# Kernel tuning notes

Hardware: AMD Instinct MI355X
Metric: run time of the kernel (lower is better)

The kernel has to match this reference:

```python
import jax, jax.numpy as jnp
import numpy as np

N, D_IN, H, E = 8192, 2048, 1024, 8

def setup_inputs() -> dict:
    key = jax.random.key(0)
    ks = jax.random.split(key, 12)
    s = lambda k, shp, fan: jax.random.normal(k, shp, jnp.float32) * (1.0 / np.sqrt(fan))
    return {
        "x": jax.random.normal(ks[0], (N, D_IN), jnp.float32),
        "enc_W": s(ks[1], (D_IN, H), D_IN),
        "enc_b": jnp.zeros((H,), jnp.float32),
        "gate_W": s(ks[2], (H, E), H),
        "expert_W": s(ks[3], (E, H, H), H),
        "expert_b": jnp.zeros((E, H), jnp.float32),
        "mlp_W": s(ks[4], (H, H), H),
        "mlp_b": jnp.zeros((H,), jnp.float32),
        "coef_W": s(ks[5], (H, 2), H),
        "coef_b": jnp.zeros((2,), jnp.float32),
        "dec_W": s(ks[6], (H, D_IN), H),
        "dec_b": jnp.zeros((D_IN,), jnp.float32),
    }

def reference(x, enc_W, enc_b, gate_W, expert_W, expert_b,
              mlp_W, mlp_b, coef_W, coef_b, dec_W, dec_b):
    # encoder + relu
    h = jax.nn.relu(x @ enc_W + enc_b)                       # [N,H]
    # top-1 gate
    probs = jax.nn.softmax(h @ gate_W, axis=-1)              # [N,E]
    idx = jnp.argmax(probs, axis=-1)                         # [N]
    p = jnp.take_along_axis(probs, idx[:, None], axis=1)     # [N,1]
    onehot = jax.nn.one_hot(idx, probs.shape[-1], dtype=h.dtype)  # [N,E]
    # dispatch -> per-expert GEMM -> combine
    xe = jnp.einsum('ne,nh->enh', onehot, h)                 # [E,N,H]
    ye = jnp.einsum('enh,ehd->end', xe, expert_W) + expert_b[:, None, :]
    moe_out = jnp.einsum('ne,end->nd', onehot, ye) * p       # [N,H]
    # residual MoE mixing
    mlp_out = h @ mlp_W + mlp_b                              # [N,H]
    coef = jax.nn.softmax(h @ coef_W + coef_b, axis=-1)      # [N,2]
    out = moe_out * coef[:, 0:1] + mlp_out * coef[:, 1:2]
    # decoder
    return out @ dec_W + dec_b                               # [N,D_IN]
```

## Files before the change

kernel.cpp:

```cpp
#include <hip/hip_runtime.h>
#include <hip/hip_bf16.h>
#include <stdint.h>


using bf16 = __hip_bfloat16;
typedef __bf16 bf16x8 __attribute__((ext_vector_type(8)));
typedef float f32x4 __attribute__((ext_vector_type(4)));

static constexpr int NROWS = 8192;
static constexpr int DIN   = 2048;
static constexpr int HD    = 1024;
static constexpr int NEXP  = 8;
static constexpr int MAX_TILES = 72;
static constexpr int MAXFLAG  = 512;
static constexpr int MAXFLAG2 = 128;
static constexpr int F1Z = 7;
#define GAPTHR  0.02f
#define GAPTHR2 1.0e-3

__device__ __forceinline__ uint16_t f2u(float f) {
  bf16 h = __float2bfloat16(f);
  uint16_t u; __builtin_memcpy(&u, &h, 2); return u;
}
__device__ __forceinline__ float u2f(uint16_t u) {
  uint32_t x = ((uint32_t)u) << 16;
  float f; __builtin_memcpy(&f, &x, 4); return f;
}

typedef const __attribute__((address_space(1))) void* gas_ptr;
typedef __attribute__((address_space(3))) void* las_ptr;
__device__ __forceinline__ void async16(void* lds, const void* g) {
  __builtin_amdgcn_global_load_lds((gas_ptr)g, (las_ptr)lds, 16, 0, 0);
}

__global__ __launch_bounds__(256)
void prep_kernel(const float* __restrict__ x, uint16_t* __restrict__ x_bf,
                 const float* __restrict__ encW, uint16_t* __restrict__ encWT,
                 const float* __restrict__ mlpW, uint16_t* __restrict__ mlpWT,
                 const float* __restrict__ decW, uint16_t* __restrict__ decWT,
                 const float* __restrict__ expW, uint16_t* __restrict__ expWT,
                 int* __restrict__ ctrs_i)
{
  __shared__ float tile[64 * 65];
  const int b = blockIdx.x;
  const int t = threadIdx.x;
  if (b == 0 && t < 64) ctrs_i[t] = 0;

  if (b < 1024) {
    for (int i = b * 256 + t; i < NROWS * DIN / 8; i += 1024 * 256) {
      const float* s = x + (size_t)i * 8;
      float4 v0 = *(const float4*)(s);
      float4 v1 = *(const float4*)(s + 4);
      uint16_t tmp[8];
      tmp[0]=f2u(v0.x); tmp[1]=f2u(v0.y); tmp[2]=f2u(v0.z); tmp[3]=f2u(v0.w);
      tmp[4]=f2u(v1.x); tmp[5]=f2u(v1.y); tmp[6]=f2u(v1.z); tmp[7]=f2u(v1.w);
      int4 pv; __builtin_memcpy(&pv, tmp, 16);
      *(int4*)(x_bf + (size_t)i * 8) = pv;
    }
    return;
  }
  const float* in; uint16_t* out; int R, C, bx, by;
  int q = b - 1024;
  if (q < 512)       { in = encW; out = encWT; R = DIN; C = HD;  bx = q & 15; by = q >> 4; }
  else if (q < 768)  { q -= 512;  in = mlpW; out = mlpWT; R = HD; C = HD;  bx = q & 15; by = q >> 4; }
  else if (q < 1280) { q -= 768;  in = decW; out = decWT; R = HD; C = DIN; bx = q & 31; by = q >> 5; }
  else { q -= 1280; const int z = q >> 8; q &= 255;
         in = expW + (size_t)z * HD * HD; out = expWT + (size_t)z * HD * HD;
         R = HD; C = HD; bx = q & 15; by = q >> 4; }
  const int C0 = bx * 64, R0 = by * 64;
  const int cl = (t & 7) * 8;
#pragma unroll
  for (int p = 0; p < 2; ++p) {
    const int r = p * 32 + (t >> 3);
    const float* src = in + (size_t)(R0 + r) * C + C0 + cl;
    float4 v0 = *(const float4*)(src);
    float4 v1 = *(const float4*)(src + 4);
    float* dst = &tile[r * 65 + cl];
    dst[0]=v0.x; dst[1]=v0.y; dst[2]=v0.z; dst[3]=v0.w;
    dst[4]=v1.x; dst[5]=v1.y; dst[6]=v1.z; dst[7]=v1.w;
  }
  __syncthreads();
#pragma unroll
  for (int p = 0; p < 2; ++p) {
    const int oc = p * 32 + (t >> 3);
    uint16_t tmp[8];
#pragma unroll
    for (int j = 0; j < 8; ++j) tmp[j] = f2u(tile[(cl + j) * 65 + oc]);
    int4 v; __builtin_memcpy(&v, tmp, 16);
    *(int4*)(out + (size_t)(C0 + oc) * R + R0 + cl) = v;
  }
}

template<int MODE>
__device__ __forceinline__
void gemm8p_body(const uint16_t* __restrict__ A, const uint16_t* __restrict__ BT,
                 uint16_t* __restrict__ C16, float* __restrict__ C32,
                 const float* __restrict__ biasf, const float* __restrict__ scale,
                 int M, int N, int K)
{
  constexpr int BM = 256, BN = 128, BK = 64;
  __shared__ uint16_t As[2][BM * BK];
  __shared__ uint16_t Bs[2][BN * BK];

  const int t = threadIdx.x;
  const int ntyg = gridDim.y;
  const int nwg  = gridDim.x * ntyg;
  const int hwf  = blockIdx.y * gridDim.x + blockIdx.x;
  const int swzb = (hwf & 7) * (nwg >> 3) + (hwf >> 3);
  const int mtile = swzb / ntyg;
  const int ntile = swzb % ntyg;

  const int trow = t >> 3;
  const int cbD  = (t & 7) * 16;
  const int cbS  = cbD ^ ((trow & 7) << 4);
  const char* aRow[4];
  const char* bRow[2];
#pragma unroll
  for (int c = 0; c < 4; ++c)
    aRow[c] = (const char*)A + ((size_t)(mtile * BM + c * 64 + trow) * K) * 2 + cbS;
#pragma unroll
  for (int c = 0; c < 2; ++c)
    bRow[c] = (const char*)BT + ((size_t)(ntile * BN + c * 64 + trow) * K) * 2 + cbS;

  auto stage = [&](int b, int kt) {
#pragma unroll
    for (int c = 0; c < 4; ++c)
      async16(&As[b][c * 4096 + t * 8], aRow[c] + (size_t)kt * 128);
#pragma unroll
    for (int c = 0; c < 2; ++c)
      async16(&Bs[b][c * 4096 + t * 8], bRow[c] + (size_t)kt * 128);
  };

  const int wid = t >> 6, lane = t & 63;
  const int wm = wid >> 2, wn = wid & 3;
  const int frow = lane & 15, hi = lane >> 4;

  f32x4 acc[8][2];
  const f32x4 zero = {0.f, 0.f, 0.f, 0.f};
#pragma unroll
  for (int i = 0; i < 8; ++i) { acc[i][0] = zero; acc[i][1] = zero; }

  auto ldfrag = [&](const uint16_t* base, int row, int kk) {
    const int cb = (kk * 64 + hi * 16) ^ ((row & 7) << 4);
    return *reinterpret_cast<const bf16x8*>(
        reinterpret_cast<const char*>(base) + row * 128 + cb);
  };

  const int nt = K >> 6;
  stage(0, 0);
  stage(1, 1);

  for (int kt = 0; kt < nt; ++kt) {
    const int b = kt & 1;
    asm volatile("s_waitcnt vmcnt(6)" ::: "memory");
    __builtin_amdgcn_s_barrier();

    bf16x8 af[8][2], bfr[2][2];
#pragma unroll
    for (int mi = 0; mi < 8; ++mi)
#pragma unroll
      for (int kk = 0; kk < 2; ++kk)
        af[mi][kk] = ldfrag(As[b], wm * 128 + mi * 16 + frow, kk);
#pragma unroll
    for (int ni = 0; ni < 2; ++ni)
#pragma unroll
      for (int kk = 0; kk < 2; ++kk)
        bfr[ni][kk] = ldfrag(Bs[b], wn * 32 + ni * 16 + frow, kk);

    asm volatile("s_waitcnt lgkmcnt(0)" ::: "memory");
    __builtin_amdgcn_s_barrier();

    if (kt + 2 < nt) stage(b, kt + 2);

    __builtin_amdgcn_s_setprio(1);
#pragma unroll
    for (int kk = 0; kk < 2; ++kk)
#pragma unroll
      for (int mi = 0; mi < 8; ++mi)
#pragma unroll
        for (int ni = 0; ni < 2; ++ni)
          acc[mi][ni] = __builtin_amdgcn_mfma_f32_16x16x32_bf16(
              af[mi][kk], bfr[ni][kk], acc[mi][ni], 0, 0, 0);
    __builtin_amdgcn_s_setprio(0);
  }

  const int nbase = ntile * BN + wn * 32;
  const int rbase = mtile * BM + wm * 128 + hi * 4;
  const int cbase = lane & 15;
#pragma unroll
  for (int mi = 0; mi < 8; ++mi) {
#pragma unroll
    for (int j = 0; j < 4; ++j) {
      const int gr = rbase + mi * 16 + j;
#pragma unroll
      for (int ni = 0; ni < 2; ++ni) {
        const int gc = nbase + ni * 16 + cbase;
        float v = acc[mi][ni][j] + biasf[gc];
        if constexpr (MODE == 0) {
          C16[(size_t)gr * N + gc] = f2u(fmaxf(v, 0.f));
        } else if constexpr (MODE == 2) {
          const float prev = u2f(C16[(size_t)gr * N + gc]);
          C16[(size_t)gr * N + gc] = f2u(prev + v * scale[gr]);
        } else {
          C32[(size_t)gr * N + gc] = v;
        }
      }
    }
  }
}

__global__ __launch_bounds__(512)
void gemm_enc(const uint16_t* A, const uint16_t* BT, uint16_t* C16,
              const float* biasf, int M, int N, int K) {
  gemm8p_body<0>(A, BT, C16, nullptr, biasf, nullptr, M, N, K);
}
__global__ __launch_bounds__(512)
void gemm_mlp(const uint16_t* A, const uint16_t* BT, uint16_t* C16,
              const float* biasf, const float* scale, int M, int N, int K) {
  gemm8p_body<2>(A, BT, C16, nullptr, biasf, scale, M, N, K);
}
__global__ __launch_bounds__(512)
void gemm_dec(const uint16_t* A, const uint16_t* BT, float* C32,
              const float* biasf, int M, int N, int K) {
  gemm8p_body<3>(A, BT, nullptr, C32, biasf, nullptr, M, N, K);
}

__global__ __launch_bounds__(256)
void gemm_moe(const uint16_t* __restrict__ A, const uint16_t* __restrict__ BT,
              uint16_t* __restrict__ C16, const float* __restrict__ biasf,
              const int* __restrict__ rowperm, const int* __restrict__ tinfo,
              const float* __restrict__ scale, int M, int N, int K)
{
  __shared__ uint16_t As[2][128 * 64];
  __shared__ uint16_t Bs[2][128 * 64];

  const int t = threadIdx.x;
  const int nty = gridDim.y;
  const int nwg = gridDim.x * nty;
  const int hwf = blockIdx.y * gridDim.x + blockIdx.x;
  const int swz = (hwf & 7) * (nwg >> 3) + (hwf >> 3);
  const int mtile = swz / nty;
  const int ntile = swz % nty;

  const int nt2 = tinfo[0];
  if (mtile >= nt2) return;
  const int e      = tinfo[1 + mtile * 3 + 0];
  const int row0   = tinfo[1 + mtile * 3 + 1];
  const int rowend = tinfo[1 + mtile * 3 + 2];

  const int kcol = (t & 7) * 8;
  const uint16_t* asrc[4];
  const uint16_t* bsrc[4];
#pragma unroll
  for (int c = 0; c < 4; ++c) {
    const int r = c * 32 + (t >> 3);
    int pr = row0 + r;
    if (pr > rowend - 1) pr = rowend - 1;
    asrc[c] = A + (size_t)rowperm[pr] * K + kcol;
    bsrc[c] = BT + ((size_t)e * N + ntile * 128 + r) * (size_t)K + kcol;
  }

  f32x4 acc[4][4];
  const f32x4 zero = {0.f, 0.f, 0.f, 0.f};
#pragma unroll
  for (int i = 0; i < 4; ++i)
#pragma unroll
    for (int j = 0; j < 4; ++j) acc[i][j] = zero;

  const int wid = t >> 6, lane = t & 63;
  const int wm = wid >> 1, wn = wid & 1;
  const int frow = lane & 15;
  const int fk = (lane >> 4) * 8;

  const int nk = K >> 6;
#pragma unroll
  for (int c = 0; c < 4; ++c) {
    async16(&As[0][c * 2048 + t * 8], asrc[c]);
    async16(&Bs[0][c * 2048 + t * 8], bsrc[c]);
  }
  __syncthreads();

  int cur = 0;
  for (int kt = 0; kt < nk; ++kt) {
    if (kt + 1 < nk) {
#pragma unroll
      for (int c = 0; c < 4; ++c) {
        async16(&As[cur ^ 1][c * 2048 + t * 8], asrc[c] + (kt + 1) * 64);
        async16(&Bs[cur ^ 1][c * 2048 + t * 8], bsrc[c] + (kt + 1) * 64);
      }
    }
#pragma unroll
    for (int kk = 0; kk < 2; ++kk) {
      bf16x8 af[4], bfr[4];
#pragma unroll
      for (int mi = 0; mi < 4; ++mi)
        af[mi] = *reinterpret_cast<const bf16x8*>(
            &As[cur][(wm * 64 + mi * 16 + frow) * 64 + kk * 32 + fk]);
#pragma unroll
      for (int ni = 0; ni < 4; ++ni)
        bfr[ni] = *reinterpret_cast<const bf16x8*>(
            &Bs[cur][(wn * 64 + ni * 16 + frow) * 64 + kk * 32 + fk]);
#pragma unroll
      for (int mi = 0; mi < 4; ++mi)
#pragma unroll
        for (int ni = 0; ni < 4; ++ni)
          acc[mi][ni] = __builtin_amdgcn_mfma_f32_16x16x32_bf16(
              af[mi], bfr[ni], acc[mi][ni], 0, 0, 0);
    }
    __syncthreads();
    cur ^= 1;
  }

  const int nbase = ntile * 128 + wn * 64;
  const int rbase = wm * 64 + (lane >> 4) * 4;
  const int cbase = lane & 15;
#pragma unroll
  for (int mi = 0; mi < 4; ++mi) {
#pragma unroll
    for (int j = 0; j < 4; ++j) {
      const int pr = row0 + rbase + mi * 16 + j;
      if (pr < rowend) {
        const int orig = rowperm[pr];
        const float sc = scale[orig];
        uint16_t* dst = C16 + (size_t)orig * N;
#pragma unroll
        for (int ni = 0; ni < 4; ++ni) {
          const int gc = nbase + ni * 16 + cbase;
          dst[gc] = f2u((acc[mi][ni][j] + biasf[e * N + gc]) * sc);
        }
      }
    }
  }
}

__global__ __launch_bounds__(256)
void gate_kernel(const uint16_t* __restrict__ hbf, const float* __restrict__ gW,
                 const float* __restrict__ cW, const float* __restrict__ cb,
                 int* __restrict__ eidx, float* __restrict__ s0,
                 float* __restrict__ c1, int* __restrict__ nflag,
                 int* __restrict__ flaglist)
{
  const int lane = threadIdx.x & 63;
  const int row  = blockIdx.x * 4 + (threadIdx.x >> 6);
  const uint16_t* hrow = hbf + (size_t)row * HD;
  float a[10];
#pragma unroll
  for (int i = 0; i < 10; ++i) a[i] = 0.f;
  for (int kk = 0; kk < HD / 64; ++kk) {
    const int k = kk * 64 + lane;
    const float hv = u2f(hrow[k]);
    float4 g0 = *(const float4*)(gW + (size_t)k * 8);
    float4 g1 = *(const float4*)(gW + (size_t)k * 8 + 4);
    a[0] += hv * g0.x; a[1] += hv * g0.y; a[2] += hv * g0.z; a[3] += hv * g0.w;
    a[4] += hv * g1.x; a[5] += hv * g1.y; a[6] += hv * g1.z; a[7] += hv * g1.w;
    float2 cv = *(const float2*)(cW + (size_t)k * 2);
    a[8] += hv * cv.x; a[9] += hv * cv.y;
  }
#pragma unroll
  for (int off = 32; off > 0; off >>= 1) {
#pragma unroll
    for (int i = 0; i < 10; ++i) a[i] += __shfl_xor(a[i], off);
  }
  if (lane == 0) {
    int best = 0; float bm = a[0];
#pragma unroll
    for (int e2 = 1; e2 < 8; ++e2) if (a[e2] > bm) { bm = a[e2]; best = e2; }
    float sec = -3.0e38f;
#pragma unroll
    for (int e2 = 0; e2 < 8; ++e2) if (e2 != best) sec = fmaxf(sec, a[e2]);
    float s = 0.f;
#pragma unroll
    for (int e2 = 0; e2 < 8; ++e2) s += expf(a[e2] - bm);
    const float p  = 1.f / s;
    const float l0 = a[8] + cb[0], l1 = a[9] + cb[1];
    const float mx = fmaxf(l0, l1);
    const float e0 = expf(l0 - mx), e1 = expf(l1 - mx);
    const float inv = 1.f / (e0 + e1);
    eidx[row] = best;
    s0[row]   = p * (e0 * inv);
    c1[row]   = e1 * inv;
    if (bm - sec < GAPTHR) {
      int fi = atomicAdd(nflag, 1);
      if (fi < MAXFLAG) flaglist[fi] = row;
    }
  }
}

template<typename T>
__global__ __launch_bounds__(256)
void fixup1_kernel(const float* __restrict__ x, const float* __restrict__ encW,
                   const int* __restrict__ flaglist, const int* __restrict__ nflag,
                   T* __restrict__ zpart, int fstride, int maxflag)
{
  __shared__ float xs[8][128];
  __shared__ T red[8][4][64];
  int nf = *nflag; if (nf > maxflag) nf = maxflag;
  if (nf <= 0) return;
  const int rs = blockIdx.z;
  const int nb = (nf + 7) >> 3;
  if (rs >= nb) return;
  const int t  = threadIdx.x;
  const int jb = blockIdx.x, kb = blockIdx.y;
  const int tj = t & 63, tk = t >> 6;
  const int j  = jb * 64 + tj;
  const int k0 = kb * 128 + tk * 32;
  float w[32];
#pragma unroll
  for (int kk = 0; kk < 32; ++kk)
    w[kk] = encW[(size_t)(k0 + kk) * HD + j];

  for (int fb = rs; fb < nb; fb += F1Z) {
    __syncthreads();
    {
      const int r  = t >> 5;
      const int kc = (t & 31) * 4;
      int f = fb * 8 + r; if (f > nf - 1) f = nf - 1;
      const int row = flaglist[f];
      *(float4*)&xs[r][kc] =
          *(const float4*)&x[(size_t)row * DIN + kb * 128 + kc];
    }
    __syncthreads();
    T acc[8];
#pragma unroll
    for (int r = 0; r < 8; ++r) acc[r] = (T)0;
#pragma unroll
    for (int kq = 0; kq < 8; ++kq) {
      float4 xv[8];
#pragma unroll
      for (int r = 0; r < 8; ++r)
        xv[r] = *(const float4*)&xs[r][tk * 32 + kq * 4];
#pragma unroll
      for (int r = 0; r < 8; ++r) {
        acc[r] += (T)xv[r].x * (T)w[kq * 4 + 0];
        acc[r] += (T)xv[r].y * (T)w[kq * 4 + 1];
        acc[r] += (T)xv[r].z * (T)w[kq * 4 + 2];
        acc[r] += (T)xv[r].w * (T)w[kq * 4 + 3];
      }
    }
#pragma unroll
    for (int r = 0; r < 8; ++r) red[r][tk][tj] = acc[r];
    __syncthreads();
#pragma unroll
    for (int p = 0; p < 2; ++p) {
      const int idx = p * 256 + t;
      const int r = idx >> 6, jj = idx & 63;
      const int f = fb * 8 + r;
      if (f < nf)
        zpart[((size_t)kb * fstride + f) * HD + jb * 64 + jj] =
            (red[r][0][jj] + red[r][1][jj]) + (red[r][2][jj] + red[r][3][jj]);
    }
  }
}

template<int STAGE, typename T>
__global__ __launch_bounds__(256)
void fixup2_kernel(const T* __restrict__ zpart, const float* __restrict__ encB,
                   const float* __restrict__ gW, const float* __restrict__ cW,
                   const float* __restrict__ cb, const int* __restrict__ flaglist,
                   const int* __restrict__ nflag, int* __restrict__ eidx,
                   float* __restrict__ s0, float* __restrict__ c1,
                   int* __restrict__ nflag2, int* __restrict__ flaglist2,
                   int fstride, int maxflag)
{
  __shared__ double red[4][10];
  int nf = *nflag; if (nf > maxflag) nf = maxflag;
  const int t = threadIdx.x, lane = t & 63, w = t >> 6;
  for (int f = blockIdx.x; f < nf; f += 128) {
    const int row = flaglist[f];
    double part[10];
#pragma unroll
    for (int i = 0; i < 10; ++i) part[i] = 0.0;
    for (int jj = t; jj < HD; jj += 256) {
      double z = 0.0;
#pragma unroll
      for (int kb = 0; kb < 16; ++kb)
        z += (double)zpart[((size_t)kb * fstride + f) * HD + jj];
      double hj = z + (double)encB[jj];
      hj = hj > 0.0 ? hj : 0.0;
      const float* gr = gW + (size_t)jj * 8;
#pragma unroll
      for (int e2 = 0; e2 < 8; ++e2) part[e2] += hj * (double)gr[e2];
      part[8] += hj * (double)cW[jj * 2];
      part[9] += hj * (double)cW[jj * 2 + 1];
    }
#pragma unroll
    for (int off = 32; off > 0; off >>= 1)
#pragma unroll
      for (int i = 0; i < 10; ++i) part[i] += __shfl_xor(part[i], off);
    if (lane == 0)
#pragma unroll
      for (int i = 0; i < 10; ++i) red[w][i] = part[i];
    __syncthreads();
    if (t == 0) {
      double a[10];
#pragma unroll
      for (int i = 0; i < 10; ++i)
        a[i] = red[0][i] + red[1][i] + red[2][i] + red[3][i];
      int best = 0; double bm = a[0];
#pragma unroll
      for (int e2 = 1; e2 < 8; ++e2) if (a[e2] > bm) { bm = a[e2]; best = e2; }
      double sec = -1.0e300;
#pragma unroll
      for (int e2 = 0; e2 < 8; ++e2) if (e2 != best && a[e2] > sec) sec = a[e2];
      double s = 0.0;
#pragma unroll
      for (int e2 = 0; e2 < 8; ++e2) s += exp(a[e2] - bm);
      const double p  = 1.0 / s;
      const double l0 = a[8] + (double)cb[0], l1 = a[9] + (double)cb[1];
      const double mx = l0 > l1 ? l0 : l1;
      const double e0 = exp(l0 - mx), e1 = exp(l1 - mx);
      const double inv = 1.0 / (e0 + e1);
      eidx[row] = best;
      s0[row]   = (float)(p * e0 * inv);
      c1[row]   = (float)(e1 * inv);
      if constexpr (STAGE == 0) {
        if (bm - sec < GAPTHR2) {
          int fi = atomicAdd(nflag2, 1);
          if (fi < MAXFLAG2) flaglist2[fi] = row;
        }
      }
    }
    __syncthreads();
  }
}

__global__ __launch_bounds__(1024)
void scan_scatter_kernel(const int* __restrict__ eidx,
                         int* __restrict__ tinfo, int* __restrict__ rowperm)
{
  __shared__ int scnt[NEXP];
  __shared__ int soffs[NEXP];
  __shared__ int scur[NEXP];
  const int t = threadIdx.x;
  if (t < NEXP) scnt[t] = 0;
  __syncthreads();
  for (int n = t; n < NROWS; n += 1024)
    atomicAdd(&scnt[eidx[n]], 1);
  __syncthreads();
  if (t == 0) {
    int off = 0, nt = 0;
    for (int e = 0; e < NEXP; ++e) {
      soffs[e] = off; scur[e] = 0;
      const int c = scnt[e];
      const int end = off + c;
      for (int r = 0; r < c; r += 128) {
        tinfo[1 + nt * 3 + 0] = e;
        tinfo[1 + nt * 3 + 1] = off + r;
        tinfo[1 + nt * 3 + 2] = end;
        ++nt;
      }
      off = end;
    }
    tinfo[0] = nt;
  }
  __syncthreads();
  for (int n = t; n < NROWS; n += 1024) {
    const int e = eidx[n];
    rowperm[soffs[e] + atomicAdd(&scur[e], 1)] = n;
  }
}

extern "C" void kernel_launch(void* const* d_in, const int* in_sizes, int n_in,
                              void* d_out, int out_size, void* d_ws, size_t ws_size,
                              hipStream_t stream) {
  (void)in_sizes; (void)n_in; (void)out_size;
  const float* x      = (const float*)d_in[0];
  const float* enc_W  = (const float*)d_in[1];
  const float* enc_b  = (const float*)d_in[2];
  const float* gate_W = (const float*)d_in[3];
  const float* exp_W  = (const float*)d_in[4];
  const float* exp_b  = (const float*)d_in[5];
  const float* mlp_W  = (const float*)d_in[6];
  const float* mlp_b  = (const float*)d_in[7];
  const float* coef_W = (const float*)d_in[8];
  const float* coef_b = (const float*)d_in[9];
  const float* dec_W  = (const float*)d_in[10];
  const float* dec_b  = (const float*)d_in[11];

  char* ws = (char*)d_ws;
  size_t off = 0;
  auto alloc = [&](size_t bytes) {
    char* p = ws + off;
    off += (bytes + 255) & ~(size_t)255;
    return p;
  };
  uint16_t* encWT  = (uint16_t*)alloc((size_t)DIN * HD * 2);
  uint16_t* mlpWT  = (uint16_t*)alloc((size_t)HD * HD * 2);
  uint16_t* decWT  = (uint16_t*)alloc((size_t)HD * DIN * 2);
  uint16_t* expWT  = (uint16_t*)alloc((size_t)NEXP * HD * HD * 2);
  uint16_t* h_bf   = (uint16_t*)alloc((size_t)NROWS * HD * 2);
  float*    zpart  = (float*)   alloc((size_t)16 * MAXFLAG * HD * 4);
  int*      eidx   = (int*)     alloc(NROWS * 4);
  float*    s0     = (float*)   alloc(NROWS * 4);
  float*    c1     = (float*)   alloc(NROWS * 4);
  int*      rowperm= (int*)     alloc(NROWS * 4);
  int*      flags  = (int*)     alloc(MAXFLAG * 4);
  int*      flags2 = (int*)     alloc(MAXFLAG2 * 4);
  char*     ctrs   = (char*)    alloc(256);
  int*      tinfo  = (int*)     alloc((1 + MAX_TILES * 3) * 4 + 64);
  uint16_t* x_bf   = (uint16_t*)zpart;
  double*   zpartB = (double*)zpart;
  uint16_t* accout = (uint16_t*)zpart;
  int*      nflag  = (int*)(ctrs + 32);
  int*      nflag2 = (int*)(ctrs + 64);
  if (off > ws_size) return;

  const dim3 blk(256);
  prep_kernel<<<dim3(4352), blk, 0, stream>>>(
      x, x_bf, enc_W, encWT, mlp_W, mlpWT, dec_W, decWT, exp_W, expWT,
      (int*)ctrs);

  gemm_enc<<<dim3(NROWS / 256, HD / 128), dim3(512), 0, stream>>>(
      x_bf, encWT, h_bf, enc_b, NROWS, HD, DIN);

  gate_kernel<<<dim3(NROWS / 4), blk, 0, stream>>>(
      h_bf, gate_W, coef_W, coef_b, eidx, s0, c1, nflag, flags);

  fixup1_kernel<float><<<dim3(16, 16, F1Z), blk, 0, stream>>>(
      x, enc_W, flags, nflag, zpart, MAXFLAG, MAXFLAG);
  fixup2_kernel<0, float><<<dim3(128), blk, 0, stream>>>(
      zpart, enc_b, gate_W, coef_W, coef_b, flags, nflag, eidx, s0, c1,
      nflag2, flags2, MAXFLAG, MAXFLAG);
  fixup1_kernel<double><<<dim3(16, 16, F1Z), blk, 0, stream>>>(
      x, enc_W, flags2, nflag2, zpartB, MAXFLAG2, MAXFLAG2);
  fixup2_kernel<1, double><<<dim3(128), blk, 0, stream>>>(
      zpartB, enc_b, gate_W, coef_W, coef_b, flags2, nflag2, eidx, s0, c1,
      nullptr, nullptr, MAXFLAG2, MAXFLAG2);

  scan_scatter_kernel<<<dim3(1), dim3(1024), 0, stream>>>(
      eidx, tinfo, rowperm);

  gemm_moe<<<dim3(MAX_TILES, HD / 128), blk, 0, stream>>>(
      h_bf, expWT, accout, exp_b, rowperm, tinfo, s0, NROWS, HD, HD);
  gemm_mlp<<<dim3(NROWS / 256, HD / 128), dim3(512), 0, stream>>>(
      h_bf, mlpWT, accout, mlp_b, c1, NROWS, HD, HD);
  gemm_dec<<<dim3(NROWS / 256, DIN / 128), dim3(512), 0, stream>>>(
      accout, decWT, (float*)d_out, dec_b, NROWS, DIN, HD);
}
```

Before: 291.7 us.

## Swizzle LDS tiles and deepen async prefetch in expert GEMM

The expert GEMM now stores its A/B tiles in LDS with an XOR swizzle on 16-byte chunks, to cut LDS bank conflicts on fragment reads. The double-buffered pipeline is restructured: two stages are prefetched up front, and each iteration waits with a vmcnt counter instead of a full syncthreads. All fragments are loaded into registers before the buffer is refilled two steps ahead. The MFMA block is wrapped in raised wave priority. The vmcnt(8) wait may not cover the final iteration, when only one stage is still in flight, which risks a read-before-arrival race.

```diff
diff --git a/kernel.cpp b/kernel.cpp
--- a/kernel.cpp
+++ b/kernel.cpp
@@ -248,17 +248,27 @@
   const int row0   = tinfo[1 + mtile * 3 + 1];
   const int rowend = tinfo[1 + mtile * 3 + 2];
 
-  const int kcol = (t & 7) * 8;
-  const uint16_t* asrc[4];
-  const uint16_t* bsrc[4];
+  const int trow = t >> 3;
+  const int cbD  = (t & 7) * 16;
+  const int cbS  = cbD ^ ((trow & 7) << 4);
+  const char* asrc[4];
+  const char* bsrc[4];
 #pragma unroll
   for (int c = 0; c < 4; ++c) {
-    const int r = c * 32 + (t >> 3);
+    const int r = c * 32 + trow;
     int pr = row0 + r;
     if (pr > rowend - 1) pr = rowend - 1;
-    asrc[c] = A + (size_t)rowperm[pr] * K + kcol;
-    bsrc[c] = BT + ((size_t)e * N + ntile * 128 + r) * (size_t)K + kcol;
-  }
+    asrc[c] = (const char*)A + ((size_t)rowperm[pr] * K) * 2 + cbS;
+    bsrc[c] = (const char*)BT + (((size_t)e * N + ntile * 128 + r) * K) * 2 + cbS;
+  }
+
+  auto stage = [&](int b, int kt) {
+#pragma unroll
+    for (int c = 0; c < 4; ++c) {
+      async16(&As[b][c * 2048 + t * 8], asrc[c] + (size_t)kt * 128);
+      async16(&Bs[b][c * 2048 + t * 8], bsrc[c] + (size_t)kt * 128);
+    }
+  };
 
   f32x4 acc[4][4];
   const f32x4 zero = {0.f, 0.f, 0.f, 0.f};
@@ -269,50 +279,54 @@
 
   const int wid = t >> 6, lane = t & 63;
   const int wm = wid >> 1, wn = wid & 1;
-  const int frow = lane & 15;
-  const int fk = (lane >> 4) * 8;
+  const int frow = lane & 15, hi = lane >> 4;
+
+  auto ldfrag = [&](const uint16_t* base, int row, int kk) {
+    const int cb = (kk * 64 + hi * 16) ^ ((row & 7) << 4);
+    return *reinterpret_cast<const bf16x8*>(
+        reinterpret_cast<const char*>(base) + row * 128 + cb);
+  };
 
   const int nk = K >> 6;
-#pragma unroll
-  for (int c = 0; c < 4; ++c) {
-    async16(&As[0][c * 2048 + t * 8], asrc[c]);
-    async16(&Bs[0][c * 2048 + t * 8], bsrc[c]);
-  }
-  __syncthreads();
-
-  int cur = 0;
+  stage(0, 0);
+  stage(1, 1);
+
   for (int kt = 0; kt < nk; ++kt) {
-    if (kt + 1 < nk) {
-#pragma unroll
-      for (int c = 0; c < 4; ++c) {
-        async16(&As[cur ^ 1][c * 2048 + t * 8], asrc[c] + (kt + 1) * 64);
-        async16(&Bs[cur ^ 1][c * 2048 + t * 8], bsrc[c] + (kt + 1) * 64);
-      }
-    }
-#pragma unroll
-    for (int kk = 0; kk < 2; ++kk) {
-      bf16x8 af[4], bfr[4];
-#pragma unroll
-      for (int mi = 0; mi < 4; ++mi)
-        af[mi] = *reinterpret_cast<const bf16x8*>(
-            &As[cur][(wm * 64 + mi * 16 + frow) * 64 + kk * 32 + fk]);
-#pragma unroll
-      for (int ni = 0; ni < 4; ++ni)
-        bfr[ni] = *reinterpret_cast<const bf16x8*>(
-            &Bs[cur][(wn * 64 + ni * 16 + frow) * 64 + kk * 32 + fk]);
+    const int b = kt & 1;
+    asm volatile("s_waitcnt vmcnt(8)" ::: "memory");
+    __builtin_amdgcn_s_barrier();
+
+    bf16x8 af[4][2], bfr[4][2];
+#pragma unroll
+    for (int mi = 0; mi < 4; ++mi)
+#pragma unroll
+      for (int kk = 0; kk < 2; ++kk)
+        af[mi][kk] = ldfrag(As[b], wm * 64 + mi * 16 + frow, kk);
+#pragma unroll
+    for (int ni = 0; ni < 4; ++ni)
+#pragma unroll
+      for (int kk = 0; kk < 2; ++kk)
+        bfr[ni][kk] = ldfrag(Bs[b], wn * 64 + ni * 16 + frow, kk);
+
+    asm volatile("s_waitcnt lgkmcnt(0)" ::: "memory");
+    __builtin_amdgcn_s_barrier();
+
+    if (kt + 2 < nk) stage(b, kt + 2);
+
+    __builtin_amdgcn_s_setprio(1);
+#pragma unroll
+    for (int kk = 0; kk < 2; ++kk)
 #pragma unroll
       for (int mi = 0; mi < 4; ++mi)
 #pragma unroll
         for (int ni = 0; ni < 4; ++ni)
           acc[mi][ni] = __builtin_amdgcn_mfma_f32_16x16x32_bf16(
-              af[mi], bfr[ni], acc[mi][ni], 0, 0, 0);
-    }
-    __syncthreads();
-    cur ^= 1;
+              af[mi][kk], bfr[ni][kk], acc[mi][ni], 0, 0, 0);
+    __builtin_amdgcn_s_setprio(0);
   }
 
   const int nbase = ntile * 128 + wn * 64;
-  const int rbase = wm * 64 + (lane >> 4) * 4;
+  const int rbase = wm * 64 + hi * 4;
   const int cbase = lane & 15;
 #pragma unroll
   for (int mi = 0; mi < 4; ++mi) {
```

Result: faster. 282.7 us (-3.1%).
